# Optimization experiments

Hardware: AMD Instinct MI355X
Metric: run time of the kernel (lower is better)

Reference implementation:

```python
import jax, jax.numpy as jnp
import numpy as np
from jax import lax

B, L, DM = 2, 1024, 1024
DIN, DSTATE, DCONV, DTRANK = 2048, 16, 4, 64


def setup_inputs() -> dict:
    key = jax.random.key(0)
    ks = jax.random.split(key, 8)
    s = 0.02
    x = jax.random.normal(ks[0], (B, L, DM), jnp.float32)
    in_proj_w = jax.random.normal(ks[1], (2 * DIN, DM), jnp.float32) * s
    conv_w = jax.random.normal(ks[2], (DIN, 1, DCONV), jnp.float32) * 0.2
    conv_b = jnp.zeros((DIN,), jnp.float32)
    x_proj_w = jax.random.normal(ks[3], (DTRANK + 2 * DSTATE, DIN), jnp.float32) * s
    dt_proj_w = jax.random.normal(ks[4], (DIN, DTRANK), jnp.float32) * s
    dt_proj_b = jnp.full((DIN,), -4.0, jnp.float32)  # small init dt after softplus
    # S4D-real init: A_log = log(1..d_state) per channel
    A_log = jnp.log(jnp.broadcast_to(jnp.arange(1, DSTATE + 1, dtype=jnp.float32), (DIN, DSTATE)))
    D_skip = jnp.ones((DIN,), jnp.float32)
    out_proj_w = jax.random.normal(ks[5], (DM, DIN), jnp.float32) * s
    return {
        "x": x, "norm_w": jnp.ones((DM,), jnp.float32), "norm_b": jnp.zeros((DM,), jnp.float32),
        "in_proj_w": in_proj_w, "conv_w": conv_w, "conv_b": conv_b,
        "x_proj_w": x_proj_w, "dt_proj_w": dt_proj_w, "dt_proj_b": dt_proj_b,
        "A_log": A_log, "D_skip": D_skip, "out_proj_w": out_proj_w,
    }


def _layernorm(x, w, b, eps=1e-5):
    mu = jnp.mean(x, axis=-1, keepdims=True)
    var = jnp.mean(jnp.square(x - mu), axis=-1, keepdims=True)
    return (x - mu) * lax.rsqrt(var + eps) * w + b


def _mamba(h, in_proj_w, conv_w, conv_b, x_proj_w, dt_proj_w, dt_proj_b, A_log, D_skip, out_proj_w):
    # h: [B, L, DM]
    xz = jnp.einsum('bld,ed->ble', h, in_proj_w)          # [B, L, 2*DIN]
    xm, z = jnp.split(xz, 2, axis=-1)                     # each [B, L, DIN]
    # causal depthwise conv1d over time
    xc = jnp.transpose(xm, (0, 2, 1))                     # [B, DIN, L]
    xc = jnp.pad(xc, ((0, 0), (0, 0), (DCONV - 1, 0)))
    xc = lax.conv_general_dilated(xc, conv_w, (1,), 'VALID',
                                  dimension_numbers=('NCH', 'OIH', 'NCH'),
                                  feature_group_count=DIN)
    xc = xc + conv_b[None, :, None]
    xc = jnp.transpose(xc, (0, 2, 1))                     # [B, L, DIN]
    xc = jax.nn.silu(xc)
    # input-dependent SSM parameters
    x_dbl = jnp.einsum('bld,ed->ble', xc, x_proj_w)       # [B, L, DTRANK+2N]
    dt, Bm, Cm = jnp.split(x_dbl, [DTRANK, DTRANK + DSTATE], axis=-1)
    dt = jax.nn.softplus(jnp.einsum('blr,dr->bld', dt, dt_proj_w) + dt_proj_b)  # [B, L, DIN]
    A = -jnp.exp(A_log)                                   # [DIN, N]
    deltaA = jnp.exp(dt[..., None] * A)                   # [B, L, DIN, N]
    deltaBu = dt[..., None] * Bm[:, :, None, :] * xc[..., None]  # [B, L, DIN, N]
    # sequential selective scan over time
    dA_t = jnp.transpose(deltaA, (1, 0, 2, 3))            # [L, B, DIN, N]
    dBu_t = jnp.transpose(deltaBu, (1, 0, 2, 3))
    C_t = jnp.transpose(Cm, (1, 0, 2))                    # [L, B, N]

    def step(hs, inp):
        dA, dBu, Ct = inp
        hs = dA * hs + dBu                                # [B, DIN, N]
        y = jnp.einsum('bdn,bn->bd', hs, Ct)
        return hs, y

    h0 = jnp.zeros((B, DIN, DSTATE), xc.dtype)
    _, ys = lax.scan(step, h0, (dA_t, dBu_t, C_t))        # ys: [L, B, DIN]
    y = jnp.transpose(ys, (1, 0, 2)) + xc * D_skip        # [B, L, DIN]
    y = y * jax.nn.silu(z)
    return jnp.einsum('bld,ed->ble', y, out_proj_w)       # [B, L, DM]


def reference(x, norm_w, norm_b, in_proj_w, conv_w, conv_b, x_proj_w,
              dt_proj_w, dt_proj_b, A_log, D_skip, out_proj_w):
    h = _layernorm(x, norm_w, norm_b)
    return x + _mamba(h, in_proj_w, conv_w, conv_b, x_proj_w,
                      dt_proj_w, dt_proj_b, A_log, D_skip, out_proj_w)
```

## Files before the change

kernel.cpp:

```cpp
#include <hip/hip_runtime.h>


typedef unsigned short u16;
typedef unsigned int u32;

typedef __bf16 bf16x8 __attribute__((ext_vector_type(8)));
typedef float f32x4 __attribute__((ext_vector_type(4)));

#define SCAN_G 32
#define SCAN_T 32
#define NSTATE 65536

#if __has_builtin(__builtin_amdgcn_exp2f)
#define EXP2F(x) __builtin_amdgcn_exp2f(x)
#else
#define EXP2F(x) exp2f(x)
#endif
#define LOG2E 1.44269504f

__device__ __forceinline__ u16 f2bf(float f) {
  u32 u = __float_as_uint(f);
  u32 r = u + 0x7FFFu + ((u >> 16) & 1u);
  return (u16)(r >> 16);
}
__device__ __forceinline__ float bf2f(u16 v) {
  return __uint_as_float(((u32)v) << 16);
}

__device__ __forceinline__ void lds_load16(const u16* g, u16* l) {
  __builtin_amdgcn_global_load_lds(
      (const __attribute__((address_space(1))) u32*)g,
      (__attribute__((address_space(3))) u32*)l, 16, 0, 0);
}

__global__ __launch_bounds__(256) void convert_ln_kernel(
    const float* __restrict__ w0, const float* __restrict__ w1,
    const float* __restrict__ w2, const float* __restrict__ w3,
    u16* __restrict__ o0, u16* __restrict__ o1,
    u16* __restrict__ o2, u16* __restrict__ o3,
    const float* __restrict__ x, const float* __restrict__ nw,
    const float* __restrict__ nb, u16* __restrict__ h) {
  const int bx = blockIdx.x;
  const int tid = threadIdx.x;
  if (bx < 25856) {
    const int i = bx * 256 + tid;
    if (i < 4194304) {
      o0[i] = f2bf(w0[i]);
    } else if (i < 4390912) {
      const int j = i - 4194304;
      o1[j] = f2bf(w1[j]);
    } else if (i < 4521984) {
      const int j = i - 4390912;
      o2[j] = f2bf(w2[j]);
    } else if (i < 6619136) {
      const int j = i - 4521984;
      o3[j] = f2bf(w3[j]);
    }
    return;
  }
  const int row = bx - 25856;
  const float4 v = ((const float4*)(x + (size_t)row * 1024))[tid];
  float s = v.x + v.y + v.z + v.w;
  float s2 = v.x * v.x + v.y * v.y + v.z * v.z + v.w * v.w;
  for (int off = 32; off >= 1; off >>= 1) {
    s += __shfl_xor(s, off);
    s2 += __shfl_xor(s2, off);
  }
  __shared__ float red[8];
  const int wave = tid >> 6;
  if ((tid & 63) == 0) { red[wave * 2] = s; red[wave * 2 + 1] = s2; }
  __syncthreads();
  s = red[0] + red[2] + red[4] + red[6];
  s2 = red[1] + red[3] + red[5] + red[7];
  const float mu = s * (1.0f / 1024.0f);
  const float var = s2 * (1.0f / 1024.0f) - mu * mu;
  const float rstd = rsqrtf(var + 1e-5f);
  const float4 wv = ((const float4*)nw)[tid];
  const float4 bv = ((const float4*)nb)[tid];
  ushort4 o;
  o.x = f2bf((v.x - mu) * rstd * wv.x + bv.x);
  o.y = f2bf((v.y - mu) * rstd * wv.y + bv.y);
  o.z = f2bf((v.z - mu) * rstd * wv.z + bv.z);
  o.w = f2bf((v.w - mu) * rstd * wv.w + bv.w);
  ((ushort4*)(h + (size_t)row * 1024))[tid] = o;
}

__global__ __launch_bounds__(256) void gemm_bt_kernel(
    const u16* __restrict__ A, const u16* __restrict__ W,
    float* __restrict__ C, int M, int N, int K) {
  const int n0 = blockIdx.x * 64;
  const int m0 = blockIdx.y * 64;
  const int ks = blockIdx.z;
  const int kLen = K / 4;
  const int kOff = ks * kLen;
  __shared__ u16 As[64 * 32];
  __shared__ u16 Ws[64 * 32];
  const int tid = threadIdx.x;
  const int wave = tid >> 6;
  const int lane = tid & 63;
  const int wm = (wave >> 1) * 32;
  const int wn = (wave & 1) * 32;
  const int lrow = tid >> 2;
  const int lcg = (tid & 3) * 8;
  const int arow = m0 + lrow;
  const int wrow = n0 + lrow;
  f32x4 acc[2][2];
#pragma unroll
  for (int i = 0; i < 2; ++i)
#pragma unroll
    for (int j = 0; j < 2; ++j) acc[i][j] = (f32x4){0.f, 0.f, 0.f, 0.f};

  const int fm = lane & 15;
  const int fk = (lane >> 4) * 8;

  for (int k0 = kOff; k0 < kOff + kLen; k0 += 32) {
    uint4 av = *(const uint4*)(A + (size_t)arow * K + k0 + lcg);
    uint4 wv = make_uint4(0u, 0u, 0u, 0u);
    if (wrow < N) wv = *(const uint4*)(W + (size_t)wrow * K + k0 + lcg);
    __syncthreads();
    *(uint4*)(As + lrow * 32 + lcg) = av;
    *(uint4*)(Ws + lrow * 32 + lcg) = wv;
    __syncthreads();
    bf16x8 a0 = *(const bf16x8*)(As + (wm + fm) * 32 + fk);
    bf16x8 a1 = *(const bf16x8*)(As + (wm + 16 + fm) * 32 + fk);
    bf16x8 b0 = *(const bf16x8*)(Ws + (wn + fm) * 32 + fk);
    bf16x8 b1 = *(const bf16x8*)(Ws + (wn + 16 + fm) * 32 + fk);
    acc[0][0] = __builtin_amdgcn_mfma_f32_16x16x32_bf16(a0, b0, acc[0][0], 0, 0, 0);
    acc[0][1] = __builtin_amdgcn_mfma_f32_16x16x32_bf16(a0, b1, acc[0][1], 0, 0, 0);
    acc[1][0] = __builtin_amdgcn_mfma_f32_16x16x32_bf16(a1, b0, acc[1][0], 0, 0, 0);
    acc[1][1] = __builtin_amdgcn_mfma_f32_16x16x32_bf16(a1, b1, acc[1][1], 0, 0, 0);
  }

  const int col = lane & 15;
  const int rbase = (lane >> 4) * 4;
#pragma unroll
  for (int tm = 0; tm < 2; ++tm)
#pragma unroll
    for (int tn = 0; tn < 2; ++tn)
#pragma unroll
      for (int r = 0; r < 4; ++r) {
        int m = m0 + wm + tm * 16 + rbase + r;
        int n = n0 + wn + tn * 16 + col;
        if (n < N)
          C[(size_t)ks * M * N + (size_t)m * N + n] = acc[tm][tn][r];
      }
}

__global__ __launch_bounds__(256) void dtgemm_fused_kernel(
    const float* __restrict__ xpart, const u16* __restrict__ Wdt,
    const float* __restrict__ bias, const u16* __restrict__ xcb,
    u32* __restrict__ dxp, float* __restrict__ xdbl) {
  const int N = 2048, K = 64;
  const int n0 = blockIdx.x * 64;
  const int m0 = blockIdx.y * 64;
  const int tid = threadIdx.x;

  if (blockIdx.x == 0) {
#pragma unroll
    for (int j = 0; j < 8; ++j) {
      const int e = tid * 8 + j;
      const int r = e >> 5, c = e & 31;
      const size_t ix = (size_t)(m0 + r) * 96 + 64 + c;
      xdbl[ix] = xpart[ix] + xpart[ix + 196608] + xpart[ix + 2 * 196608] +
                 xpart[ix + 3 * 196608];
    }
  }

  __shared__ u16 As[64 * 32];
  __shared__ u16 Ws[64 * 32];
  const int wave = tid >> 6;
  const int lane = tid & 63;
  const int wm = (wave >> 1) * 32;
  const int wn = (wave & 1) * 32;
  const int lrow = tid >> 2;
  const int lcg = (tid & 3) * 8;
  f32x4 acc[2][2];
#pragma unroll
  for (int i = 0; i < 2; ++i)
#pragma unroll
    for (int j = 0; j < 2; ++j) acc[i][j] = (f32x4){0.f, 0.f, 0.f, 0.f};

  const int fm = lane & 15;
  const int fk = (lane >> 4) * 8;

  for (int k0 = 0; k0 < K; k0 += 32) {
    const size_t ab = (size_t)(m0 + lrow) * 96 + k0 + lcg;
    float av[8];
#pragma unroll
    for (int t = 0; t < 2; ++t) {
      float4 v0 = *(const float4*)&xpart[ab + t * 4];
      float4 v1 = *(const float4*)&xpart[ab + 196608 + t * 4];
      float4 v2 = *(const float4*)&xpart[ab + 2 * 196608 + t * 4];
      float4 v3 = *(const float4*)&xpart[ab + 3 * 196608 + t * 4];
      av[t * 4 + 0] = v0.x + v1.x + v2.x + v3.x;
      av[t * 4 + 1] = v0.y + v1.y + v2.y + v3.y;
      av[t * 4 + 2] = v0.z + v1.z + v2.z + v3.z;
      av[t * 4 + 3] = v0.w + v1.w + v2.w + v3.w;
    }
    ushort4 ap0, ap1;
    ap0.x = f2bf(av[0]); ap0.y = f2bf(av[1]); ap0.z = f2bf(av[2]); ap0.w = f2bf(av[3]);
    ap1.x = f2bf(av[4]); ap1.y = f2bf(av[5]); ap1.z = f2bf(av[6]); ap1.w = f2bf(av[7]);
    uint4 wv = *(const uint4*)(Wdt + (size_t)(n0 + lrow) * K + k0 + lcg);
    __syncthreads();
    *(ushort4*)(As + lrow * 32 + lcg) = ap0;
    *(ushort4*)(As + lrow * 32 + lcg + 4) = ap1;
    *(uint4*)(Ws + lrow * 32 + lcg) = wv;
    __syncthreads();
    bf16x8 a0 = *(const bf16x8*)(As + (wm + fm) * 32 + fk);
    bf16x8 a1 = *(const bf16x8*)(As + (wm + 16 + fm) * 32 + fk);
    bf16x8 b0 = *(const bf16x8*)(Ws + (wn + fm) * 32 + fk);
    bf16x8 b1 = *(const bf16x8*)(Ws + (wn + 16 + fm) * 32 + fk);
    acc[0][0] = __builtin_amdgcn_mfma_f32_16x16x32_bf16(a0, b0, acc[0][0], 0, 0, 0);
    acc[0][1] = __builtin_amdgcn_mfma_f32_16x16x32_bf16(a0, b1, acc[0][1], 0, 0, 0);
    acc[1][0] = __builtin_amdgcn_mfma_f32_16x16x32_bf16(a1, b0, acc[1][0], 0, 0, 0);
    acc[1][1] = __builtin_amdgcn_mfma_f32_16x16x32_bf16(a1, b1, acc[1][1], 0, 0, 0);
  }

  const int col = lane & 15;
  const int rbase = (lane >> 4) * 4;
#pragma unroll
  for (int tm = 0; tm < 2; ++tm)
#pragma unroll
    for (int tn = 0; tn < 2; ++tn)
#pragma unroll
      for (int r = 0; r < 4; ++r) {
        const int m = m0 + wm + tm * 16 + rbase + r;
        const int n = n0 + wn + tn * 16 + col;
        float v = acc[tm][tn][r] + bias[n];
        v = (v > 20.f) ? v : log1pf(__expf(v));
        const u32 xc = xcb[(size_t)m * 2048 + n];
        dxp[(size_t)m * 2048 + n] = (u32)f2bf(v) | (xc << 16);
      }
}

template <int EPI, int SPLITK>
__global__ __launch_bounds__(256) void gemm128_kernel(
    const u16* __restrict__ A, const u16* __restrict__ W,
    u16* __restrict__ Cout, int M, int N, int K) {
  const int n0 = blockIdx.x * 128;
  const int m0 = blockIdx.y * 128;
  const int ks = (SPLITK > 1) ? blockIdx.z : 0;
  const int kLen = K / SPLITK;
  const int k0 = ks * kLen;
  __shared__ u16 As[128 * 32];
  __shared__ u16 Ws[128 * 32];
  const int tid = threadIdx.x;
  const int wave = tid >> 6;
  const int lane = tid & 63;
  const int wm = (wave >> 1) * 64;
  const int wn = (wave & 1) * 64;
  f32x4 acc[4][4];
#pragma unroll
  for (int i = 0; i < 4; ++i)
#pragma unroll
    for (int j = 0; j < 4; ++j) acc[i][j] = (f32x4){0.f, 0.f, 0.f, 0.f};

  const int fm = lane & 15;
  const int fk = (lane >> 4) * 8;
  const int sr = lane >> 2;
  const int sc = (lane & 3) * 8;
  const u16* gA = A + (size_t)(m0 + wave * 32 + sr) * K + k0 + sc;
  const u16* gB = W + (size_t)(n0 + wave * 32 + sr) * K + k0 + sc;
  u16* lA = As + wave * 1024;
  u16* lB = Ws + wave * 1024;

  for (int kk = 0; kk < kLen; kk += 32) {
    __syncthreads();
    lds_load16(gA + kk, lA);
    lds_load16(gA + (size_t)16 * K + kk, lA + 512);
    lds_load16(gB + kk, lB);
    lds_load16(gB + (size_t)16 * K + kk, lB + 512);
    __syncthreads();
    bf16x8 af[4], bfr[4];
#pragma unroll
    for (int i = 0; i < 4; ++i)
      af[i] = *(const bf16x8*)(As + (wm + i * 16 + fm) * 32 + fk);
#pragma unroll
    for (int j = 0; j < 4; ++j)
      bfr[j] = *(const bf16x8*)(Ws + (wn + j * 16 + fm) * 32 + fk);
#pragma unroll
    for (int i = 0; i < 4; ++i)
#pragma unroll
      for (int j = 0; j < 4; ++j)
        acc[i][j] = __builtin_amdgcn_mfma_f32_16x16x32_bf16(af[i], bfr[j], acc[i][j], 0, 0, 0);
  }

  const int col = lane & 15;
  const int rb = (lane >> 4) * 4;
#pragma unroll
  for (int i = 0; i < 4; ++i)
#pragma unroll
    for (int j = 0; j < 4; ++j)
#pragma unroll
      for (int r = 0; r < 4; ++r) {
        const int m = m0 + wm + i * 16 + rb + r;
        const int n = n0 + wn + j * 16 + col;
        if (EPI == 4)
          Cout[(size_t)m * N + n] = f2bf(acc[i][j][r]);
        else
          Cout[(size_t)ks * M * N + (size_t)m * N + n] = f2bf(acc[i][j][r]);
      }
}

__global__ __launch_bounds__(256) void out_comb_kernel(
    const u16* __restrict__ part, const float* __restrict__ x,
    float* __restrict__ out) {
  const int i4 = (blockIdx.x * 256 + threadIdx.x) * 4;
  const float4 xv = *(const float4*)&x[i4];
  float a0 = xv.x, a1 = xv.y, a2 = xv.z, a3 = xv.w;
#pragma unroll
  for (int ks = 0; ks < 4; ++ks) {
    ushort4 pv = *(const ushort4*)&part[(size_t)ks * 2097152 + i4];
    a0 += bf2f(pv.x); a1 += bf2f(pv.y); a2 += bf2f(pv.z); a3 += bf2f(pv.w);
  }
  float4 o = {a0, a1, a2, a3};
  *(float4*)&out[i4] = o;
}

__global__ __launch_bounds__(256) void conv_silu_kernel(
    const u16* __restrict__ xzb, const float* __restrict__ cw,
    const float* __restrict__ cb, u16* __restrict__ xcb) {
  const int idx = blockIdx.x * 256 + threadIdx.x;
  const int d = idx & 2047;
  const int m = idx >> 11;
  const int l = m & 1023;
  const float4 wv = ((const float4*)cw)[d];
  const float w4[4] = {wv.x, wv.y, wv.z, wv.w};
  float acc = cb[d];
#pragma unroll
  for (int k = 0; k < 4; ++k) {
    int lk = l + k - 3;
    if (lk >= 0) acc += bf2f(xzb[(size_t)(m + k - 3) * 4096 + d]) * w4[k];
  }
  const float sv = acc / (1.0f + __expf(-acc));
  xcb[idx] = f2bf(sv);
}

__global__ __launch_bounds__(256) void scan_pass1_kernel(
    const u32* __restrict__ dxp, const float* __restrict__ xdbl,
    const float* __restrict__ A_log, float* __restrict__ hend,
    float* __restrict__ prodA) {
  const int bx = blockIdx.x;
  const int d0 = (bx & 7) * 256;
  const int b = (bx >> 3) & 1;
  const int g = bx >> 4;
  const int tid = threadIdx.x;
  const int d = d0 + tid;
  const int mb = b * 1024 + g * SCAN_T;

  float a2[16];
#pragma unroll
  for (int q = 0; q < 4; ++q) {
    float4 al = *(const float4*)&A_log[(size_t)d * 16 + q * 4];
    a2[q * 4 + 0] = -__expf(al.x) * LOG2E;
    a2[q * 4 + 1] = -__expf(al.y) * LOG2E;
    a2[q * 4 + 2] = -__expf(al.z) * LOG2E;
    a2[q * 4 + 3] = -__expf(al.w) * LOG2E;
  }

  float h[16];
#pragma unroll
  for (int n = 0; n < 16; ++n) h[n] = 0.f;
  float cs = 0.f;

  const u32* dp = dxp + (size_t)mb * 2048 + d;
  const float* xb = xdbl + (size_t)mb * 96 + 64;

#pragma unroll 4
  for (int s = 0; s < SCAN_T; ++s) {
    const u32 u = dp[(size_t)s * 2048];
    const float dtv = __uint_as_float(u << 16);
    const float xcv = __uint_as_float(u & 0xFFFF0000u);
    const float du = dtv * xcv;
    const float4 B0 = *(const float4*)(xb + (size_t)s * 96 + 0);
    const float4 B1 = *(const float4*)(xb + (size_t)s * 96 + 4);
    const float4 B2 = *(const float4*)(xb + (size_t)s * 96 + 8);
    const float4 B3 = *(const float4*)(xb + (size_t)s * 96 + 12);
    const float Bv[16] = {B0.x, B0.y, B0.z, B0.w, B1.x, B1.y, B1.z, B1.w,
                          B2.x, B2.y, B2.z, B2.w, B3.x, B3.y, B3.z, B3.w};
#pragma unroll
    for (int n = 0; n < 16; ++n) {
      const float da = EXP2F(dtv * a2[n]);
      h[n] = __builtin_fmaf(da, h[n], du * Bv[n]);
    }
    cs += dtv;
  }

  const size_t base = ((size_t)(g * 2 + b) * 2048 + d) * 16;
#pragma unroll
  for (int q = 0; q < 4; ++q) {
    float4 hv = {h[q * 4], h[q * 4 + 1], h[q * 4 + 2], h[q * 4 + 3]};
    *(float4*)&hend[base + q * 4] = hv;
    float4 pv = {EXP2F(a2[q * 4] * cs), EXP2F(a2[q * 4 + 1] * cs),
                 EXP2F(a2[q * 4 + 2] * cs), EXP2F(a2[q * 4 + 3] * cs)};
    *(float4*)&prodA[base + q * 4] = pv;
  }
}

__global__ __launch_bounds__(256) void scan_combine_kernel(
    const float* __restrict__ hend, const float* __restrict__ prodA,
    float* __restrict__ hinit) {
  const int sid = blockIdx.x * 256 + threadIdx.x;
  float H = 0.f;
#pragma unroll 8
  for (int g = 0; g < SCAN_G; ++g) {
    hinit[g * NSTATE + sid] = H;
    H = prodA[g * NSTATE + sid] * H + hend[g * NSTATE + sid];
  }
}

__global__ __launch_bounds__(256) void scan_pass2_kernel(
    const u32* __restrict__ dxp, const u16* __restrict__ xzb,
    const float* __restrict__ xdbl, const float* __restrict__ A_log,
    const float* __restrict__ Dsk, const float* __restrict__ hinit,
    u16* __restrict__ yb) {
  const int bx = blockIdx.x;
  const int d0 = (bx & 7) * 256;
  const int b = (bx >> 3) & 1;
  const int g = bx >> 4;
  const int tid = threadIdx.x;
  const int d = d0 + tid;
  const int mb = b * 1024 + g * SCAN_T;

  float a2[16];
#pragma unroll
  for (int q = 0; q < 4; ++q) {
    float4 al = *(const float4*)&A_log[(size_t)d * 16 + q * 4];
    a2[q * 4 + 0] = -__expf(al.x) * LOG2E;
    a2[q * 4 + 1] = -__expf(al.y) * LOG2E;
    a2[q * 4 + 2] = -__expf(al.z) * LOG2E;
    a2[q * 4 + 3] = -__expf(al.w) * LOG2E;
  }
  const float Dd = Dsk[d];

  float h[16];
  {
    const float* hi = hinit + ((size_t)(g * 2 + b) * 2048 + d) * 16;
#pragma unroll
    for (int q = 0; q < 4; ++q) {
      float4 hv = *(const float4*)(hi + q * 4);
      h[q * 4] = hv.x; h[q * 4 + 1] = hv.y; h[q * 4 + 2] = hv.z; h[q * 4 + 3] = hv.w;
    }
  }

  const u32* dp = dxp + (size_t)mb * 2048 + d;
  const u16* zp = xzb + (size_t)mb * 4096 + 2048 + d;
  const float* xb = xdbl + (size_t)mb * 96 + 64;
  u16* yp = yb + (size_t)mb * 2048 + d;

#pragma unroll 2
  for (int s = 0; s < SCAN_T; ++s) {
    const u32 u = dp[(size_t)s * 2048];
    const float dtv = __uint_as_float(u << 16);
    const float xcv = __uint_as_float(u & 0xFFFF0000u);
    const float du = dtv * xcv;
    const float4 B0 = *(const float4*)(xb + (size_t)s * 96 + 0);
    const float4 B1 = *(const float4*)(xb + (size_t)s * 96 + 4);
    const float4 B2 = *(const float4*)(xb + (size_t)s * 96 + 8);
    const float4 B3 = *(const float4*)(xb + (size_t)s * 96 + 12);
    const float4 C0 = *(const float4*)(xb + (size_t)s * 96 + 16);
    const float4 C1 = *(const float4*)(xb + (size_t)s * 96 + 20);
    const float4 C2 = *(const float4*)(xb + (size_t)s * 96 + 24);
    const float4 C3 = *(const float4*)(xb + (size_t)s * 96 + 28);
    const float Bv[16] = {B0.x, B0.y, B0.z, B0.w, B1.x, B1.y, B1.z, B1.w,
                          B2.x, B2.y, B2.z, B2.w, B3.x, B3.y, B3.z, B3.w};
    const float Cv[16] = {C0.x, C0.y, C0.z, C0.w, C1.x, C1.y, C1.z, C1.w,
                          C2.x, C2.y, C2.z, C2.w, C3.x, C3.y, C3.z, C3.w};
    float y = 0.f;
#pragma unroll
    for (int n = 0; n < 16; ++n) {
      const float da = EXP2F(dtv * a2[n]);
      h[n] = __builtin_fmaf(da, h[n], du * Bv[n]);
      y = __builtin_fmaf(h[n], Cv[n], y);
    }
    const float zv = bf2f(zp[(size_t)s * 4096]);
    const float sig = 1.0f / (1.0f + EXP2F(-zv * LOG2E));
    const float yv = (y + xcv * Dd) * (zv * sig);
    yp[(size_t)s * 2048] = f2bf(yv);
  }
}

extern "C" void kernel_launch(void* const* d_in, const int* in_sizes, int n_in,
                              void* d_out, int out_size, void* d_ws, size_t ws_size,
                              hipStream_t stream) {
  const float* x        = (const float*)d_in[0];
  const float* norm_w   = (const float*)d_in[1];
  const float* norm_b   = (const float*)d_in[2];
  const float* in_projw = (const float*)d_in[3];
  const float* conv_w   = (const float*)d_in[4];
  const float* conv_b   = (const float*)d_in[5];
  const float* x_projw  = (const float*)d_in[6];
  const float* dt_projw = (const float*)d_in[7];
  const float* dt_projb = (const float*)d_in[8];
  const float* A_log    = (const float*)d_in[9];
  const float* D_skip   = (const float*)d_in[10];
  const float* out_projw= (const float*)d_in[11];
  float* out = (float*)d_out;

  char* p = (char*)d_ws;
  auto alloc = [&](size_t bytes) {
    char* r = p;
    p += (bytes + 255) & ~(size_t)255;
    return r;
  };
  u16* xzb    = (u16*)alloc(2048ULL * 4096 * 2);
  u16* xcb    = (u16*)alloc(2048ULL * 2048 * 2);
  u32* dxp    = (u32*)alloc(2048ULL * 2048 * 4);
  float* xdbl = (float*)alloc(2048ULL * 96 * 4);
  u16* h_bf   = (u16*)alloc(2048ULL * 1024 * 2);
  u16* ybf    = (u16*)alloc(2048ULL * 2048 * 2);
  u16* Wi     = (u16*)alloc(4096ULL * 1024 * 2);
  u16* Wx     = (u16*)alloc(96ULL * 2048 * 2);
  u16* Wdt    = (u16*)alloc(2048ULL * 64 * 2);
  u16* Wo     = (u16*)alloc(1024ULL * 2048 * 2);
  float* hend = (float*)alloc((size_t)SCAN_G * NSTATE * 4);
  float* prodA= (float*)alloc((size_t)SCAN_G * NSTATE * 4);
  float* hinit= (float*)alloc((size_t)SCAN_G * NSTATE * 4);
  float* xpart= (float*)alloc(4ULL * 2048 * 96 * 4);
  u16* opart  = xzb;
  (void)ws_size; (void)in_sizes; (void)n_in; (void)out_size;

  convert_ln_kernel<<<27904, 256, 0, stream>>>(in_projw, x_projw, dt_projw,
                                               out_projw, Wi, Wx, Wdt, Wo,
                                               x, norm_w, norm_b, h_bf);

  gemm128_kernel<4, 1><<<dim3(32, 16), 256, 0, stream>>>(h_bf, Wi, xzb, 2048, 4096, 1024);

  conv_silu_kernel<<<16384, 256, 0, stream>>>(xzb, conv_w, conv_b, xcb);

  gemm_bt_kernel<<<dim3(2, 32, 4), 256, 0, stream>>>(xcb, Wx, xpart, 2048, 96, 2048);

  dtgemm_fused_kernel<<<dim3(32, 32), 256, 0, stream>>>(xpart, Wdt, dt_projb,
                                                        xcb, dxp, xdbl);

  scan_pass1_kernel<<<512, 256, 0, stream>>>(dxp, xdbl, A_log, hend, prodA);
  scan_combine_kernel<<<256, 256, 0, stream>>>(hend, prodA, hinit);
  scan_pass2_kernel<<<512, 256, 0, stream>>>(dxp, xzb, xdbl, A_log, D_skip,
                                             hinit, ybf);

  gemm128_kernel<3, 4><<<dim3(8, 16, 4), 256, 0, stream>>>(ybf, Wo, opart, 2048, 1024, 2048);
  out_comb_kernel<<<2048, 256, 0, stream>>>(opart, x, out);
}
```

Before: 243.9 us.

## Fuse all pipeline stages into one cooperative persistent kernel with grid syncs

Replaces the ten separate kernel launches with a single cooperative mega-kernel of 512 blocks that runs every stage (weight conversion, layernorm, in-proj GEMM, conv+SiLU, x-proj GEMM, dt GEMM, two-pass scan, out-proj GEMM, residual combine) and separates them with grid.sync(). The x-proj split-K is also widened from 4 to 8 partitions. The aim is to remove per-launch overhead and inter-kernel gaps. The cost is a fixed grid size that may underuse the GPU in some stages (e.g. conv and conversion loops), grid-wide barrier latency, and a requirement of two resident blocks per CU. It falls back to the old multi-kernel path if the cooperative launch fails.

Result: no change. 245.8 us (+0.8%).

```diff
diff --git a/kernel.cpp b/kernel.cpp
--- a/kernel.cpp
+++ b/kernel.cpp
@@ -1,4 +1,7 @@
 #include <hip/hip_runtime.h>
+#include <hip/hip_cooperative_groups.h>
+
+namespace cg = cooperative_groups;
 
 
 typedef unsigned short u16;
@@ -31,6 +34,445 @@
   __builtin_amdgcn_global_load_lds(
       (const __attribute__((address_space(1))) u32*)g,
       (__attribute__((address_space(3))) u32*)l, 16, 0, 0);
+}
+
+struct MegaParams {
+  const float *x, *norm_w, *norm_b, *in_projw, *conv_w, *conv_b;
+  const float *x_projw, *dt_projw, *dt_projb, *A_log, *D_skip, *out_projw;
+  float* out;
+  u16 *xzb, *xcb, *h_bf, *ybf, *Wi, *Wx, *Wdt, *Wo;
+  u32* dxp;
+  float *xdbl, *hend, *prodA, *hinit, *xpart;
+};
+
+__device__ __forceinline__ void gemm128_body(
+    const u16* A, const u16* W, u16* Cout, int N, int K,
+    int m0, int n0, int kOff, int kLen, size_t outBase, u16* As, u16* Ws) {
+  const int tid = threadIdx.x;
+  const int wave = tid >> 6;
+  const int lane = tid & 63;
+  const int wm = (wave >> 1) * 64;
+  const int wn = (wave & 1) * 64;
+  f32x4 acc[4][4];
+#pragma unroll
+  for (int i = 0; i < 4; ++i)
+#pragma unroll
+    for (int j = 0; j < 4; ++j) acc[i][j] = (f32x4){0.f, 0.f, 0.f, 0.f};
+  const int fm = lane & 15;
+  const int fk = (lane >> 4) * 8;
+  const int sr = lane >> 2;
+  const int sc = (lane & 3) * 8;
+  const u16* gA = A + (size_t)(m0 + wave * 32 + sr) * K + kOff + sc;
+  const u16* gB = W + (size_t)(n0 + wave * 32 + sr) * K + kOff + sc;
+  u16* lA = As + wave * 1024;
+  u16* lB = Ws + wave * 1024;
+
+  for (int kk = 0; kk < kLen; kk += 32) {
+    __syncthreads();
+    lds_load16(gA + kk, lA);
+    lds_load16(gA + (size_t)16 * K + kk, lA + 512);
+    lds_load16(gB + kk, lB);
+    lds_load16(gB + (size_t)16 * K + kk, lB + 512);
+    __syncthreads();
+    bf16x8 af[4], bfr[4];
+#pragma unroll
+    for (int i = 0; i < 4; ++i)
+      af[i] = *(const bf16x8*)(As + (wm + i * 16 + fm) * 32 + fk);
+#pragma unroll
+    for (int j = 0; j < 4; ++j)
+      bfr[j] = *(const bf16x8*)(Ws + (wn + j * 16 + fm) * 32 + fk);
+#pragma unroll
+    for (int i = 0; i < 4; ++i)
+#pragma unroll
+      for (int j = 0; j < 4; ++j)
+        acc[i][j] = __builtin_amdgcn_mfma_f32_16x16x32_bf16(af[i], bfr[j], acc[i][j], 0, 0, 0);
+  }
+  const int col = lane & 15;
+  const int rb = (lane >> 4) * 4;
+#pragma unroll
+  for (int i = 0; i < 4; ++i)
+#pragma unroll
+    for (int j = 0; j < 4; ++j)
+#pragma unroll
+      for (int r = 0; r < 4; ++r) {
+        const int m = m0 + wm + i * 16 + rb + r;
+        const int n = n0 + wn + j * 16 + col;
+        Cout[outBase + (size_t)m * N + n] = f2bf(acc[i][j][r]);
+      }
+}
+
+__global__ __launch_bounds__(256, 2) void mega_kernel(MegaParams p) {
+  cg::grid_group grid = cg::this_grid();
+  __shared__ char smem_raw[16384];
+  u16* sm16 = (u16*)smem_raw;
+  const int tid = threadIdx.x;
+  const int bid = blockIdx.x;
+  const int gid = bid * 256 + tid;
+
+  for (int u = gid; u < 1654784; u += 131072) {
+    const float* src;
+    u16* dst;
+    int off;
+    if (u < 1048576) { src = p.in_projw; dst = p.Wi; off = u; }
+    else if (u < 1097728) { src = p.x_projw; dst = p.Wx; off = u - 1048576; }
+    else if (u < 1130496) { src = p.dt_projw; dst = p.Wdt; off = u - 1097728; }
+    else { src = p.out_projw; dst = p.Wo; off = u - 1130496; }
+    const float4 v = ((const float4*)src)[off];
+    ushort4 o;
+    o.x = f2bf(v.x); o.y = f2bf(v.y); o.z = f2bf(v.z); o.w = f2bf(v.w);
+    ((ushort4*)dst)[off] = o;
+  }
+  {
+    float* red = (float*)smem_raw;
+    for (int j = 0; j < 4; ++j) {
+      const int row = bid * 4 + j;
+      __syncthreads();
+      const float4 v = ((const float4*)(p.x + (size_t)row * 1024))[tid];
+      float s = v.x + v.y + v.z + v.w;
+      float s2 = v.x * v.x + v.y * v.y + v.z * v.z + v.w * v.w;
+      for (int off = 32; off >= 1; off >>= 1) {
+        s += __shfl_xor(s, off);
+        s2 += __shfl_xor(s2, off);
+      }
+      const int wave = tid >> 6;
+      if ((tid & 63) == 0) { red[wave * 2] = s; red[wave * 2 + 1] = s2; }
+      __syncthreads();
+      s = red[0] + red[2] + red[4] + red[6];
+      s2 = red[1] + red[3] + red[5] + red[7];
+      const float mu = s * (1.0f / 1024.0f);
+      const float var = s2 * (1.0f / 1024.0f) - mu * mu;
+      const float rstd = rsqrtf(var + 1e-5f);
+      const float4 wv = ((const float4*)p.norm_w)[tid];
+      const float4 bv = ((const float4*)p.norm_b)[tid];
+      ushort4 o;
+      o.x = f2bf((v.x - mu) * rstd * wv.x + bv.x);
+      o.y = f2bf((v.y - mu) * rstd * wv.y + bv.y);
+      o.z = f2bf((v.z - mu) * rstd * wv.z + bv.z);
+      o.w = f2bf((v.w - mu) * rstd * wv.w + bv.w);
+      ((ushort4*)(p.h_bf + (size_t)row * 1024))[tid] = o;
+    }
+  }
+  grid.sync();
+
+  gemm128_body(p.h_bf, p.Wi, p.xzb, 4096, 1024,
+               (bid >> 5) * 128, (bid & 31) * 128, 0, 1024, 0,
+               sm16, sm16 + 4096);
+  grid.sync();
+
+  for (int u = gid; u < 1048576; u += 131072) {
+    const int d4 = (u & 511) * 4;
+    const int m = u >> 9;
+    const int l = m & 1023;
+    float4 wv0 = ((const float4*)p.conv_w)[d4];
+    float4 wv1 = ((const float4*)p.conv_w)[d4 + 1];
+    float4 wv2 = ((const float4*)p.conv_w)[d4 + 2];
+    float4 wv3 = ((const float4*)p.conv_w)[d4 + 3];
+    const float4 cbv = ((const float4*)p.conv_b)[u & 511];
+    float a0 = cbv.x, a1 = cbv.y, a2 = cbv.z, a3 = cbv.w;
+    const float wk[4][4] = {{wv0.x, wv0.y, wv0.z, wv0.w},
+                            {wv1.x, wv1.y, wv1.z, wv1.w},
+                            {wv2.x, wv2.y, wv2.z, wv2.w},
+                            {wv3.x, wv3.y, wv3.z, wv3.w}};
+#pragma unroll
+    for (int k = 0; k < 4; ++k) {
+      if (l + k - 3 >= 0) {
+        const ushort4 xv = *(const ushort4*)&p.xzb[(size_t)(m + k - 3) * 4096 + d4];
+        a0 += bf2f(xv.x) * wk[0][k];
+        a1 += bf2f(xv.y) * wk[1][k];
+        a2 += bf2f(xv.z) * wk[2][k];
+        a3 += bf2f(xv.w) * wk[3][k];
+      }
+    }
+    ushort4 o;
+    o.x = f2bf(a0 / (1.0f + __expf(-a0)));
+    o.y = f2bf(a1 / (1.0f + __expf(-a1)));
+    o.z = f2bf(a2 / (1.0f + __expf(-a2)));
+    o.w = f2bf(a3 / (1.0f + __expf(-a3)));
+    *(ushort4*)&p.xcb[(size_t)m * 2048 + d4] = o;
+  }
+  grid.sync();
+
+  {
+    const int N = 96, K = 2048, kLen = 256;
+    const int ks = bid & 7;
+    const int n0 = ((bid >> 3) & 1) * 64;
+    const int m0 = (bid >> 4) * 64;
+    const int kOff = ks * kLen;
+    u16* As = sm16;
+    u16* Ws = sm16 + 2048;
+    const int wave = tid >> 6;
+    const int lane = tid & 63;
+    const int wm = (wave >> 1) * 32;
+    const int wn = (wave & 1) * 32;
+    const int lrow = tid >> 2;
+    const int lcg = (tid & 3) * 8;
+    f32x4 acc[2][2];
+#pragma unroll
+    for (int i = 0; i < 2; ++i)
+#pragma unroll
+      for (int j = 0; j < 2; ++j) acc[i][j] = (f32x4){0.f, 0.f, 0.f, 0.f};
+    const int fm = lane & 15;
+    const int fk = (lane >> 4) * 8;
+    const int wrow = n0 + lrow;
+    for (int k0 = kOff; k0 < kOff + kLen; k0 += 32) {
+      uint4 av = *(const uint4*)(p.xcb + (size_t)(m0 + lrow) * K + k0 + lcg);
+      uint4 wv = make_uint4(0u, 0u, 0u, 0u);
+      if (wrow < N) wv = *(const uint4*)(p.Wx + (size_t)wrow * K + k0 + lcg);
+      __syncthreads();
+      *(uint4*)(As + lrow * 32 + lcg) = av;
+      *(uint4*)(Ws + lrow * 32 + lcg) = wv;
+      __syncthreads();
+      bf16x8 a0 = *(const bf16x8*)(As + (wm + fm) * 32 + fk);
+      bf16x8 a1 = *(const bf16x8*)(As + (wm + 16 + fm) * 32 + fk);
+      bf16x8 b0 = *(const bf16x8*)(Ws + (wn + fm) * 32 + fk);
+      bf16x8 b1 = *(const bf16x8*)(Ws + (wn + 16 + fm) * 32 + fk);
+      acc[0][0] = __builtin_amdgcn_mfma_f32_16x16x32_bf16(a0, b0, acc[0][0], 0, 0, 0);
+      acc[0][1] = __builtin_amdgcn_mfma_f32_16x16x32_bf16(a0, b1, acc[0][1], 0, 0, 0);
+      acc[1][0] = __builtin_amdgcn_mfma_f32_16x16x32_bf16(a1, b0, acc[1][0], 0, 0, 0);
+      acc[1][1] = __builtin_amdgcn_mfma_f32_16x16x32_bf16(a1, b1, acc[1][1], 0, 0, 0);
+    }
+    const int col = lane & 15;
+    const int rbase = (lane >> 4) * 4;
+#pragma unroll
+    for (int tm = 0; tm < 2; ++tm)
+#pragma unroll
+      for (int tn = 0; tn < 2; ++tn)
+#pragma unroll
+        for (int r = 0; r < 4; ++r) {
+          const int m = m0 + wm + tm * 16 + rbase + r;
+          const int n = n0 + wn + tn * 16 + col;
+          if (n < N)
+            p.xpart[(size_t)ks * 196608 + (size_t)m * N + n] = acc[tm][tn][r];
+        }
+  }
+  grid.sync();
+
+  for (int t = bid * 2; t < bid * 2 + 2; ++t) {
+    const int N = 2048, K = 64;
+    const int n0 = (t & 31) * 64;
+    const int m0 = (t >> 5) * 64;
+    if ((t & 31) == 0) {
+#pragma unroll
+      for (int j = 0; j < 8; ++j) {
+        const int e = tid * 8 + j;
+        const size_t ix = (size_t)(m0 + (e >> 5)) * 96 + 64 + (e & 31);
+        float v = 0.f;
+#pragma unroll
+        for (int s = 0; s < 8; ++s) v += p.xpart[(size_t)s * 196608 + ix];
+        p.xdbl[ix] = v;
+      }
+    }
+    u16* As = sm16;
+    u16* Ws = sm16 + 2048;
+    const int wave = tid >> 6;
+    const int lane = tid & 63;
+    const int wm = (wave >> 1) * 32;
+    const int wn = (wave & 1) * 32;
+    const int lrow = tid >> 2;
+    const int lcg = (tid & 3) * 8;
+    f32x4 acc[2][2];
+#pragma unroll
+    for (int i = 0; i < 2; ++i)
+#pragma unroll
+      for (int j = 0; j < 2; ++j) acc[i][j] = (f32x4){0.f, 0.f, 0.f, 0.f};
+    const int fm = lane & 15;
+    const int fk = (lane >> 4) * 8;
+    for (int k0 = 0; k0 < K; k0 += 32) {
+      const size_t ab = (size_t)(m0 + lrow) * 96 + k0 + lcg;
+      float av[8];
+#pragma unroll
+      for (int t2 = 0; t2 < 2; ++t2) {
+        float4 sum = *(const float4*)&p.xpart[ab + t2 * 4];
+#pragma unroll
+        for (int s = 1; s < 8; ++s) {
+          const float4 vs = *(const float4*)&p.xpart[(size_t)s * 196608 + ab + t2 * 4];
+          sum.x += vs.x; sum.y += vs.y; sum.z += vs.z; sum.w += vs.w;
+        }
+        av[t2 * 4 + 0] = sum.x; av[t2 * 4 + 1] = sum.y;
+        av[t2 * 4 + 2] = sum.z; av[t2 * 4 + 3] = sum.w;
+      }
+      ushort4 ap0, ap1;
+      ap0.x = f2bf(av[0]); ap0.y = f2bf(av[1]); ap0.z = f2bf(av[2]); ap0.w = f2bf(av[3]);
+      ap1.x = f2bf(av[4]); ap1.y = f2bf(av[5]); ap1.z = f2bf(av[6]); ap1.w = f2bf(av[7]);
+      uint4 wv = *(const uint4*)(p.Wdt + (size_t)(n0 + lrow) * K + k0 + lcg);
+      __syncthreads();
+      *(ushort4*)(As + lrow * 32 + lcg) = ap0;
+      *(ushort4*)(As + lrow * 32 + lcg + 4) = ap1;
+      *(uint4*)(Ws + lrow * 32 + lcg) = wv;
+      __syncthreads();
+      bf16x8 a0 = *(const bf16x8*)(As + (wm + fm) * 32 + fk);
+      bf16x8 a1 = *(const bf16x8*)(As + (wm + 16 + fm) * 32 + fk);
+      bf16x8 b0 = *(const bf16x8*)(Ws + (wn + fm) * 32 + fk);
+      bf16x8 b1 = *(const bf16x8*)(Ws + (wn + 16 + fm) * 32 + fk);
+      acc[0][0] = __builtin_amdgcn_mfma_f32_16x16x32_bf16(a0, b0, acc[0][0], 0, 0, 0);
+      acc[0][1] = __builtin_amdgcn_mfma_f32_16x16x32_bf16(a0, b1, acc[0][1], 0, 0, 0);
+      acc[1][0] = __builtin_amdgcn_mfma_f32_16x16x32_bf16(a1, b0, acc[1][0], 0, 0, 0);
+      acc[1][1] = __builtin_amdgcn_mfma_f32_16x16x32_bf16(a1, b1, acc[1][1], 0, 0, 0);
+    }
+    const int col = lane & 15;
+    const int rbase = (lane >> 4) * 4;
+#pragma unroll
+    for (int tm = 0; tm < 2; ++tm)
+#pragma unroll
+      for (int tn = 0; tn < 2; ++tn)
+#pragma unroll
+        for (int r = 0; r < 4; ++r) {
+          const int m = m0 + wm + tm * 16 + rbase + r;
+          const int n = n0 + wn + tn * 16 + col;
+          float v = acc[tm][tn][r] + p.dt_projb[n];
+          v = (v > 20.f) ? v : log1pf(__expf(v));
+          const u32 xc = p.xcb[(size_t)m * 2048 + n];
+          p.dxp[(size_t)m * 2048 + n] = (u32)f2bf(v) | (xc << 16);
+        }
+  }
+  grid.sync();
+
+  {
+    const int d0 = (bid & 7) * 256;
+    const int b = (bid >> 3) & 1;
+    const int g = bid >> 4;
+    const int d = d0 + tid;
+    const int mb = b * 1024 + g * SCAN_T;
+    float a2[16];
+#pragma unroll
+    for (int q = 0; q < 4; ++q) {
+      float4 al = *(const float4*)&p.A_log[(size_t)d * 16 + q * 4];
+      a2[q * 4 + 0] = -__expf(al.x) * LOG2E;
+      a2[q * 4 + 1] = -__expf(al.y) * LOG2E;
+      a2[q * 4 + 2] = -__expf(al.z) * LOG2E;
+      a2[q * 4 + 3] = -__expf(al.w) * LOG2E;
+    }
+    float h[16];
+#pragma unroll
+    for (int n = 0; n < 16; ++n) h[n] = 0.f;
+    float cs = 0.f;
+    const u32* dp = p.dxp + (size_t)mb * 2048 + d;
+    const float* xb = p.xdbl + (size_t)mb * 96 + 64;
+#pragma unroll 4
+    for (int s = 0; s < SCAN_T; ++s) {
+      const u32 u = dp[(size_t)s * 2048];
+      const float dtv = __uint_as_float(u << 16);
+      const float xcv = __uint_as_float(u & 0xFFFF0000u);
+      const float du = dtv * xcv;
+      const float4 B0 = *(const float4*)(xb + (size_t)s * 96 + 0);
+      const float4 B1 = *(const float4*)(xb + (size_t)s * 96 + 4);
+      const float4 B2 = *(const float4*)(xb + (size_t)s * 96 + 8);
+      const float4 B3 = *(const float4*)(xb + (size_t)s * 96 + 12);
+      const float Bv[16] = {B0.x, B0.y, B0.z, B0.w, B1.x, B1.y, B1.z, B1.w,
+                            B2.x, B2.y, B2.z, B2.w, B3.x, B3.y, B3.z, B3.w};
+#pragma unroll
+      for (int n = 0; n < 16; ++n) {
+        const float da = EXP2F(dtv * a2[n]);
+        h[n] = __builtin_fmaf(da, h[n], du * Bv[n]);
+      }
+      cs += dtv;
+    }
+    const size_t base = ((size_t)(g * 2 + b) * 2048 + d) * 16;
+#pragma unroll
+    for (int q = 0; q < 4; ++q) {
+      float4 hv = {h[q * 4], h[q * 4 + 1], h[q * 4 + 2], h[q * 4 + 3]};
+      *(float4*)&p.hend[base + q * 4] = hv;
+      float4 pv = {EXP2F(a2[q * 4] * cs), EXP2F(a2[q * 4 + 1] * cs),
+                   EXP2F(a2[q * 4 + 2] * cs), EXP2F(a2[q * 4 + 3] * cs)};
+      *(float4*)&p.prodA[base + q * 4] = pv;
+    }
+  }
+  grid.sync();
+
+  if (gid < NSTATE) {
+    float H = 0.f;
+#pragma unroll 8
+    for (int g = 0; g < SCAN_G; ++g) {
+      p.hinit[g * NSTATE + gid] = H;
+      H = p.prodA[g * NSTATE + gid] * H + p.hend[g * NSTATE + gid];
+    }
+  }
+  grid.sync();
+
+  {
+    const int d0 = (bid & 7) * 256;
+    const int b = (bid >> 3) & 1;
+    const int g = bid >> 4;
+    const int d = d0 + tid;
+    const int mb = b * 1024 + g * SCAN_T;
+    float a2[16];
+#pragma unroll
+    for (int q = 0; q < 4; ++q) {
+      float4 al = *(const float4*)&p.A_log[(size_t)d * 16 + q * 4];
+      a2[q * 4 + 0] = -__expf(al.x) * LOG2E;
+      a2[q * 4 + 1] = -__expf(al.y) * LOG2E;
+      a2[q * 4 + 2] = -__expf(al.z) * LOG2E;
+      a2[q * 4 + 3] = -__expf(al.w) * LOG2E;
+    }
+    const float Dd = p.D_skip[d];
+    float h[16];
+    {
+      const float* hi = p.hinit + ((size_t)(g * 2 + b) * 2048 + d) * 16;
+#pragma unroll
+      for (int q = 0; q < 4; ++q) {
+        float4 hv = *(const float4*)(hi + q * 4);
+        h[q * 4] = hv.x; h[q * 4 + 1] = hv.y;
+        h[q * 4 + 2] = hv.z; h[q * 4 + 3] = hv.w;
+      }
+    }
+    const u32* dp = p.dxp + (size_t)mb * 2048 + d;
+    const u16* zp = p.xzb + (size_t)mb * 4096 + 2048 + d;
+    const float* xb = p.xdbl + (size_t)mb * 96 + 64;
+    u16* yp = p.ybf + (size_t)mb * 2048 + d;
+#pragma unroll 2
+    for (int s = 0; s < SCAN_T; ++s) {
+      const u32 u = dp[(size_t)s * 2048];
+      const float dtv = __uint_as_float(u << 16);
+      const float xcv = __uint_as_float(u & 0xFFFF0000u);
+      const float du = dtv * xcv;
+      const float4 B0 = *(const float4*)(xb + (size_t)s * 96 + 0);
+      const float4 B1 = *(const float4*)(xb + (size_t)s * 96 + 4);
+      const float4 B2 = *(const float4*)(xb + (size_t)s * 96 + 8);
+      const float4 B3 = *(const float4*)(xb + (size_t)s * 96 + 12);
+      const float4 C0 = *(const float4*)(xb + (size_t)s * 96 + 16);
+      const float4 C1 = *(const float4*)(xb + (size_t)s * 96 + 20);
+      const float4 C2 = *(const float4*)(xb + (size_t)s * 96 + 24);
+      const float4 C3 = *(const float4*)(xb + (size_t)s * 96 + 28);
+      const float Bv[16] = {B0.x, B0.y, B0.z, B0.w, B1.x, B1.y, B1.z, B1.w,
+                            B2.x, B2.y, B2.z, B2.w, B3.x, B3.y, B3.z, B3.w};
+      const float Cv[16] = {C0.x, C0.y, C0.z, C0.w, C1.x, C1.y, C1.z, C1.w,
+                            C2.x, C2.y, C2.z, C2.w, C3.x, C3.y, C3.z, C3.w};
+      float y = 0.f;
+#pragma unroll
+      for (int n = 0; n < 16; ++n) {
+        const float da = EXP2F(dtv * a2[n]);
+        h[n] = __builtin_fmaf(da, h[n], du * Bv[n]);
+        y = __builtin_fmaf(h[n], Cv[n], y);
+      }
+      const float zv = bf2f(zp[(size_t)s * 4096]);
+      const float sig = 1.0f / (1.0f + EXP2F(-zv * LOG2E));
+      const float yv = (y + xcv * Dd) * (zv * sig);
+      yp[(size_t)s * 2048] = f2bf(yv);
+    }
+  }
+  grid.sync();
+
+  {
+    const int ks = bid & 3;
+    const int n0 = ((bid >> 2) & 7) * 128;
+    const int m0 = (bid >> 5) * 128;
+    gemm128_body(p.ybf, p.Wo, p.xzb, 1024, 2048, m0, n0, ks * 512, 512,
+                 (size_t)ks * 2097152, sm16, sm16 + 4096);
+  }
+  grid.sync();
+
+  for (int u = gid; u < 524288; u += 131072) {
+    const int i4 = u * 4;
+    const float4 xv = *(const float4*)&p.x[i4];
+    float a0 = xv.x, a1 = xv.y, a2 = xv.z, a3 = xv.w;
+#pragma unroll
+    for (int ks = 0; ks < 4; ++ks) {
+      const ushort4 pv = *(const ushort4*)&p.xzb[(size_t)ks * 2097152 + i4];
+      a0 += bf2f(pv.x); a1 += bf2f(pv.y); a2 += bf2f(pv.z); a3 += bf2f(pv.w);
+    }
+    float4 o = {a0, a1, a2, a3};
+    *(float4*)&p.out[i4] = o;
+  }
 }
 
 __global__ __launch_bounds__(256) void convert_ln_kernel(
@@ -102,19 +544,16 @@
   const int wn = (wave & 1) * 32;
   const int lrow = tid >> 2;
   const int lcg = (tid & 3) * 8;
-  const int arow = m0 + lrow;
-  const int wrow = n0 + lrow;
   f32x4 acc[2][2];
 #pragma unroll
   for (int i = 0; i < 2; ++i)
 #pragma unroll
     for (int j = 0; j < 2; ++j) acc[i][j] = (f32x4){0.f, 0.f, 0.f, 0.f};
-
   const int fm = lane & 15;
   const int fk = (lane >> 4) * 8;
-
+  const int wrow = n0 + lrow;
   for (int k0 = kOff; k0 < kOff + kLen; k0 += 32) {
-    uint4 av = *(const uint4*)(A + (size_t)arow * K + k0 + lcg);
+    uint4 av = *(const uint4*)(A + (size_t)(m0 + lrow) * K + k0 + lcg);
     uint4 wv = make_uint4(0u, 0u, 0u, 0u);
     if (wrow < N) wv = *(const uint4*)(W + (size_t)wrow * K + k0 + lcg);
     __syncthreads();
@@ -130,7 +569,6 @@
     acc[1][0] = __builtin_amdgcn_mfma_f32_16x16x32_bf16(a1, b0, acc[1][0], 0, 0, 0);
     acc[1][1] = __builtin_amdgcn_mfma_f32_16x16x32_bf16(a1, b1, acc[1][1], 0, 0, 0);
   }
-
   const int col = lane & 15;
   const int rbase = (lane >> 4) * 4;
 #pragma unroll
@@ -154,18 +592,15 @@
   const int n0 = blockIdx.x * 64;
   const int m0 = blockIdx.y * 64;
   const int tid = threadIdx.x;
-
   if (blockIdx.x == 0) {
 #pragma unroll
     for (int j = 0; j < 8; ++j) {
       const int e = tid * 8 + j;
-      const int r = e >> 5, c = e & 31;
-      const size_t ix = (size_t)(m0 + r) * 96 + 64 + c;
+      const size_t ix = (size_t)(m0 + (e >> 5)) * 96 + 64 + (e & 31);
       xdbl[ix] = xpart[ix] + xpart[ix + 196608] + xpart[ix + 2 * 196608] +
                  xpart[ix + 3 * 196608];
     }
   }
-
   __shared__ u16 As[64 * 32];
   __shared__ u16 Ws[64 * 32];
   const int wave = tid >> 6;
@@ -179,10 +614,8 @@
   for (int i = 0; i < 2; ++i)
 #pragma unroll
     for (int j = 0; j < 2; ++j) acc[i][j] = (f32x4){0.f, 0.f, 0.f, 0.f};
-
   const int fm = lane & 15;
   const int fk = (lane >> 4) * 8;
-
   for (int k0 = 0; k0 < K; k0 += 32) {
     const size_t ab = (size_t)(m0 + lrow) * 96 + k0 + lcg;
     float av[8];
@@ -215,7 +648,6 @@
     acc[1][0] = __builtin_amdgcn_mfma_f32_16x16x32_bf16(a1, b0, acc[1][0], 0, 0, 0);
     acc[1][1] = __builtin_amdgcn_mfma_f32_16x16x32_bf16(a1, b1, acc[1][1], 0, 0, 0);
   }
-
   const int col = lane & 15;
   const int rbase = (lane >> 4) * 4;
 #pragma unroll
@@ -241,80 +673,10 @@
   const int m0 = blockIdx.y * 128;
   const int ks = (SPLITK > 1) ? blockIdx.z : 0;
   const int kLen = K / SPLITK;
-  const int k0 = ks * kLen;
   __shared__ u16 As[128 * 32];
   __shared__ u16 Ws[128 * 32];
-  const int tid = threadIdx.x;
-  const int wave = tid >> 6;
-  const int lane = tid & 63;
-  const int wm = (wave >> 1) * 64;
-  const int wn = (wave & 1) * 64;
-  f32x4 acc[4][4];
-#pragma unroll
-  for (int i = 0; i < 4; ++i)
-#pragma unroll
-    for (int j = 0; j < 4; ++j) acc[i][j] = (f32x4){0.f, 0.f, 0.f, 0.f};
-
-  const int fm = lane & 15;
-  const int fk = (lane >> 4) * 8;
-  const int sr = lane >> 2;
-  const int sc = (lane & 3) * 8;
-  const u16* gA = A + (size_t)(m0 + wave * 32 + sr) * K + k0 + sc;
-  const u16* gB = W + (size_t)(n0 + wave * 32 + sr) * K + k0 + sc;
-  u16* lA = As + wave * 1024;
-  u16* lB = Ws + wave * 1024;
-
-  for (int kk = 0; kk < kLen; kk += 32) {
-    __syncthreads();
-    lds_load16(gA + kk, lA);
-    lds_load16(gA + (size_t)16 * K + kk, lA + 512);
-    lds_load16(gB + kk, lB);
-    lds_load16(gB + (size_t)16 * K + kk, lB + 512);
-    __syncthreads();
-    bf16x8 af[4], bfr[4];
-#pragma unroll
-    for (int i = 0; i < 4; ++i)
-      af[i] = *(const bf16x8*)(As + (wm + i * 16 + fm) * 32 + fk);
-#pragma unroll
-    for (int j = 0; j < 4; ++j)
-      bfr[j] = *(const bf16x8*)(Ws + (wn + j * 16 + fm) * 32 + fk);
-#pragma unroll
-    for (int i = 0; i < 4; ++i)
-#pragma unroll
-      for (int j = 0; j < 4; ++j)
-        acc[i][j] = __builtin_amdgcn_mfma_f32_16x16x32_bf16(af[i], bfr[j], acc[i][j], 0, 0, 0);
-  }
-
-  const int col = lane & 15;
-  const int rb = (lane >> 4) * 4;
-#pragma unroll
-  for (int i = 0; i < 4; ++i)
-#pragma unroll
-    for (int j = 0; j < 4; ++j)
-#pragma unroll
-      for (int r = 0; r < 4; ++r) {
-        const int m = m0 + wm + i * 16 + rb + r;
-        const int n = n0 + wn + j * 16 + col;
-        if (EPI == 4)
-          Cout[(size_t)m * N + n] = f2bf(acc[i][j][r]);
-        else
-          Cout[(size_t)ks * M * N + (size_t)m * N + n] = f2bf(acc[i][j][r]);
-      }
-}
-
-__global__ __launch_bounds__(256) void out_comb_kernel(
-    const u16* __restrict__ part, const float* __restrict__ x,
-    float* __restrict__ out) {
-  const int i4 = (blockIdx.x * 256 + threadIdx.x) * 4;
-  const float4 xv = *(const float4*)&x[i4];
-  float a0 = xv.x, a1 = xv.y, a2 = xv.z, a3 = xv.w;
-#pragma unroll
-  for (int ks = 0; ks < 4; ++ks) {
-    ushort4 pv = *(const ushort4*)&part[(size_t)ks * 2097152 + i4];
-    a0 += bf2f(pv.x); a1 += bf2f(pv.y); a2 += bf2f(pv.z); a3 += bf2f(pv.w);
-  }
-  float4 o = {a0, a1, a2, a3};
-  *(float4*)&out[i4] = o;
+  gemm128_body(A, W, Cout, N, K, m0, n0, ks * kLen, kLen,
+               (EPI == 4) ? 0 : (size_t)ks * M * N, As, Ws);
 }
 
 __global__ __launch_bounds__(256) void conv_silu_kernel(
@@ -347,7 +709,6 @@
   const int tid = threadIdx.x;
   const int d = d0 + tid;
   const int mb = b * 1024 + g * SCAN_T;
-
   float a2[16];
 #pragma unroll
   for (int q = 0; q < 4; ++q) {
@@ -357,15 +718,12 @@
     a2[q * 4 + 2] = -__expf(al.z) * LOG2E;
     a2[q * 4 + 3] = -__expf(al.w) * LOG2E;
   }
-
   float h[16];
 #pragma unroll
   for (int n = 0; n < 16; ++n) h[n] = 0.f;
   float cs = 0.f;
-
   const u32* dp = dxp + (size_t)mb * 2048 + d;
   const float* xb = xdbl + (size_t)mb * 96 + 64;
-
 #pragma unroll 4
   for (int s = 0; s < SCAN_T; ++s) {
     const u32 u = dp[(size_t)s * 2048];
@@ -385,7 +743,6 @@
     }
     cs += dtv;
   }
-
   const size_t base = ((size_t)(g * 2 + b) * 2048 + d) * 16;
 #pragma unroll
   for (int q = 0; q < 4; ++q) {
@@ -421,7 +778,6 @@
   const int tid = threadIdx.x;
   const int d = d0 + tid;
   const int mb = b * 1024 + g * SCAN_T;
-
   float a2[16];
 #pragma unroll
   for (int q = 0; q < 4; ++q) {
@@ -432,7 +788,6 @@
     a2[q * 4 + 3] = -__expf(al.w) * LOG2E;
   }
   const float Dd = Dsk[d];
-
   float h[16];
   {
     const float* hi = hinit + ((size_t)(g * 2 + b) * 2048 + d) * 16;
@@ -442,12 +797,10 @@
       h[q * 4] = hv.x; h[q * 4 + 1] = hv.y; h[q * 4 + 2] = hv.z; h[q * 4 + 3] = hv.w;
     }
   }
-
   const u32* dp = dxp + (size_t)mb * 2048 + d;
   const u16* zp = xzb + (size_t)mb * 4096 + 2048 + d;
   const float* xb = xdbl + (size_t)mb * 96 + 64;
   u16* yp = yb + (size_t)mb * 2048 + d;
-
 #pragma unroll 2
   for (int s = 0; s < SCAN_T; ++s) {
     const u32 u = dp[(size_t)s * 2048];
@@ -480,64 +833,93 @@
   }
 }
 
+__global__ __launch_bounds__(256) void out_comb_kernel(
+    const u16* __restrict__ part, const float* __restrict__ x,
+    float* __restrict__ out) {
+  const int i4 = (blockIdx.x * 256 + threadIdx.x) * 4;
+  const float4 xv = *(const float4*)&x[i4];
+  float a0 = xv.x, a1 = xv.y, a2 = xv.z, a3 = xv.w;
+#pragma unroll
+  for (int ks = 0; ks < 4; ++ks) {
+    ushort4 pv = *(const ushort4*)&part[(size_t)ks * 2097152 + i4];
+    a0 += bf2f(pv.x); a1 += bf2f(pv.y); a2 += bf2f(pv.z); a3 += bf2f(pv.w);
+  }
+  float4 o = {a0, a1, a2, a3};
+  *(float4*)&out[i4] = o;
+}
+
 extern "C" void kernel_launch(void* const* d_in, const int* in_sizes, int n_in,
                               void* d_out, int out_size, void* d_ws, size_t ws_size,
                               hipStream_t stream) {
-  const float* x        = (const float*)d_in[0];
-  const float* norm_w   = (const float*)d_in[1];
-  const float* norm_b   = (const float*)d_in[2];
-  const float* in_projw = (const float*)d_in[3];
-  const float* conv_w   = (const float*)d_in[4];
-  const float* conv_b   = (const float*)d_in[5];
-  const float* x_projw  = (const float*)d_in[6];
-  const float* dt_projw = (const float*)d_in[7];
-  const float* dt_projb = (const float*)d_in[8];
-  const float* A_log    = (const float*)d_in[9];
-  const float* D_skip   = (const float*)d_in[10];
-  const float* out_projw= (const float*)d_in[11];
-  float* out = (float*)d_out;
-
-  char* p = (char*)d_ws;
+  char* pws = (char*)d_ws;
   auto alloc = [&](size_t bytes) {
-    char* r = p;
-    p += (bytes + 255) & ~(size_t)255;
+    char* r = pws;
+    pws += (bytes + 255) & ~(size_t)255;
     return r;
   };
-  u16* xzb    = (u16*)alloc(2048ULL * 4096 * 2);
-  u16* xcb    = (u16*)alloc(2048ULL * 2048 * 2);
-  u32* dxp    = (u32*)alloc(2048ULL * 2048 * 4);
-  float* xdbl = (float*)alloc(2048ULL * 96 * 4);
-  u16* h_bf   = (u16*)alloc(2048ULL * 1024 * 2);
-  u16* ybf    = (u16*)alloc(2048ULL * 2048 * 2);
-  u16* Wi     = (u16*)alloc(4096ULL * 1024 * 2);
-  u16* Wx     = (u16*)alloc(96ULL * 2048 * 2);
-  u16* Wdt    = (u16*)alloc(2048ULL * 64 * 2);
-  u16* Wo     = (u16*)alloc(1024ULL * 2048 * 2);
-  float* hend = (float*)alloc((size_t)SCAN_G * NSTATE * 4);
-  float* prodA= (float*)alloc((size_t)SCAN_G * NSTATE * 4);
-  float* hinit= (float*)alloc((size_t)SCAN_G * NSTATE * 4);
-  float* xpart= (float*)alloc(4ULL * 2048 * 96 * 4);
-  u16* opart  = xzb;
-  (void)ws_size; (void)in_sizes; (void)n_in; (void)out_size;
-
-  convert_ln_kernel<<<27904, 256, 0, stream>>>(in_projw, x_projw, dt_projw,
-                                               out_projw, Wi, Wx, Wdt, Wo,
-                                               x, norm_w, norm_b, h_bf);
-
-  gemm128_kernel<4, 1><<<dim3(32, 16), 256, 0, stream>>>(h_bf, Wi, xzb, 2048, 4096, 1024);
-
-  conv_silu_kernel<<<16384, 256, 0, stream>>>(xzb, conv_w, conv_b, xcb);
-
-  gemm_bt_kernel<<<dim3(2, 32, 4), 256, 0, stream>>>(xcb, Wx, xpart, 2048, 96, 2048);
-
-  dtgemm_fused_kernel<<<dim3(32, 32), 256, 0, stream>>>(xpart, Wdt, dt_projb,
-                                                        xcb, dxp, xdbl);
-
-  scan_pass1_kernel<<<512, 256, 0, stream>>>(dxp, xdbl, A_log, hend, prodA);
-  scan_combine_kernel<<<256, 256, 0, stream>>>(hend, prodA, hinit);
-  scan_pass2_kernel<<<512, 256, 0, stream>>>(dxp, xzb, xdbl, A_log, D_skip,
-                                             hinit, ybf);
-
-  gemm128_kernel<3, 4><<<dim3(8, 16, 4), 256, 0, stream>>>(ybf, Wo, opart, 2048, 1024, 2048);
-  out_comb_kernel<<<2048, 256, 0, stream>>>(opart, x, out);
-}
+  MegaParams mp;
+  mp.x        = (const float*)d_in[0];
+  mp.norm_w   = (const float*)d_in[1];
+  mp.norm_b   = (const float*)d_in[2];
+  mp.in_projw = (const float*)d_in[3];
+  mp.conv_w   = (const float*)d_in[4];
+  mp.conv_b   = (const float*)d_in[5];
+  mp.x_projw  = (const float*)d_in[6];
+  mp.dt_projw = (const float*)d_in[7];
+  mp.dt_projb = (const float*)d_in[8];
+  mp.A_log    = (const float*)d_in[9];
+  mp.D_skip   = (const float*)d_in[10];
+  mp.out_projw= (const float*)d_in[11];
+  mp.out      = (float*)d_out;
+  mp.xzb   = (u16*)alloc(2048ULL * 4096 * 2);
+  mp.xcb   = (u16*)alloc(2048ULL * 2048 * 2);
+  mp.dxp   = (u32*)alloc(2048ULL * 2048 * 4);
+  mp.xdbl  = (float*)alloc(2048ULL * 96 * 4);
+  mp.h_bf  = (u16*)alloc(2048ULL * 1024 * 2);
+  mp.ybf   = (u16*)alloc(2048ULL * 2048 * 2);
+  mp.Wi    = (u16*)alloc(4096ULL * 1024 * 2);
+  mp.Wx    = (u16*)alloc(96ULL * 2048 * 2);
+  mp.Wdt   = (u16*)alloc(2048ULL * 64 * 2);
+  mp.Wo    = (u16*)alloc(1024ULL * 2048 * 2);
+  mp.hend  = (float*)alloc((size_t)SCAN_G * NSTATE * 4);
+  mp.prodA = (float*)alloc((size_t)SCAN_G * NSTATE * 4);
+  mp.hinit = (float*)alloc((size_t)SCAN_G * NSTATE * 4);
+  mp.xpart = (float*)alloc(8ULL * 2048 * 96 * 4);
+  (void)in_sizes; (void)n_in; (void)out_size; (void)ws_size;
+
+  bool coop = false;
+  int maxBlocksPerCU = 0;
+  if (hipOccupancyMaxActiveBlocksPerMultiprocessor(
+          &maxBlocksPerCU, (const void*)mega_kernel, 256, 0) == hipSuccess &&
+      maxBlocksPerCU >= 2) {
+    void* args[] = {&mp};
+    if (hipLaunchCooperativeKernel((const void*)mega_kernel, dim3(512),
+                                   dim3(256), args, 0, stream) == hipSuccess)
+      coop = true;
+    else
+      (void)hipGetLastError();
+  }
+
+  if (!coop) {
+    convert_ln_kernel<<<27904, 256, 0, stream>>>(
+        mp.in_projw, mp.x_projw, mp.dt_projw, mp.out_projw,
+        mp.Wi, mp.Wx, mp.Wdt, mp.Wo, mp.x, mp.norm_w, mp.norm_b, mp.h_bf);
+    gemm128_kernel<4, 1><<<dim3(32, 16), 256, 0, stream>>>(
+        mp.h_bf, mp.Wi, mp.xzb, 2048, 4096, 1024);
+    conv_silu_kernel<<<16384, 256, 0, stream>>>(mp.xzb, mp.conv_w, mp.conv_b,
+                                                mp.xcb);
+    gemm_bt_kernel<<<dim3(2, 32, 4), 256, 0, stream>>>(mp.xcb, mp.Wx, mp.xpart,
+                                                       2048, 96, 2048);
+    dtgemm_fused_kernel<<<dim3(32, 32), 256, 0, stream>>>(
+        mp.xpart, mp.Wdt, mp.dt_projb, mp.xcb, mp.dxp, mp.xdbl);
+    scan_pass1_kernel<<<512, 256, 0, stream>>>(mp.dxp, mp.xdbl, mp.A_log,
+                                               mp.hend, mp.prodA);
+    scan_combine_kernel<<<256, 256, 0, stream>>>(mp.hend, mp.prodA, mp.hinit);
+    scan_pass2_kernel<<<512, 256, 0, stream>>>(mp.dxp, mp.xzb, mp.xdbl,
+                                               mp.A_log, mp.D_skip, mp.hinit,
+                                               mp.ybf);
+    gemm128_kernel<3, 4><<<dim3(8, 16, 4), 256, 0, stream>>>(
+        mp.ybf, mp.Wo, mp.xzb, 2048, 1024, 2048);
+    out_comb_kernel<<<2048, 256, 0, stream>>>(mp.xzb, mp.x, mp.out);
+  }
+}
```
